# Kernel tuning notes

Measured on AMD Instinct MI355X. Metric: run time of the kernel, lower is better.

The kernel has to match this reference:

```python
import jax, jax.numpy as jnp
import numpy as np

N_HEADS = 8

def setup_inputs() -> dict:
    key = jax.random.key(0)
    kq, kk, kv = jax.random.split(key, 3)
    B, L, E = 2, 2048, 512
    return {
        "queries": jax.random.normal(kq, (B, L, E), dtype=jnp.float32),
        "keys": jax.random.normal(kk, (B, L, E), dtype=jnp.float32),
        "values": jax.random.normal(kv, (B, L, E), dtype=jnp.float32),
    }

def reference(queries, keys, values):
    B, L, E = queries.shape
    H = N_HEADS
    d = E // H
    q = queries.reshape(B, L, H, d).transpose(0, 2, 1, 3)   # [B,H,L,d]
    k = keys.reshape(B, L, H, d).transpose(0, 2, 1, 3)      # [B,H,L,d]
    v = values.reshape(B, L, H, d).transpose(0, 2, 3, 1)    # [B,H,d,L]
    # FFT cross-correlation over the channel dim (faithful to source)
    q_fft = jnp.fft.rfft(q, axis=-1)
    k_fft = jnp.fft.rfft(k, axis=-1)
    corr = jnp.fft.irfft(q_fft * jnp.conj(k_fft), n=L, axis=-1)  # [B,H,L,L]
    # time_delay_agg_training
    mean_value = jnp.mean(corr, axis=1, keepdims=True)           # [B,1,L,L]
    weights = jax.nn.softmax(corr - mean_value, axis=-1)         # [B,H,L,L]
    # V = (weights^T @ v^T)^T  -> [B,H,d,L]
    Vt = jnp.einsum('bhsl,bhds->bhdl', weights, v)
    # out = V.permute(0,2,1,3).reshape(B,L,-1)  with V=[B,H,d,L]
    out = jnp.transpose(Vt, (0, 2, 1, 3)).reshape(B, L, H * d)
    return out
```

## Files before the change

kernel.cpp:

```cpp
#include <hip/hip_runtime.h>
#include <math.h>

constexpr int CL = 2048;
constexpr int NROW = 32768;
constexpr float SCALE = 1.0f / 2048.0f;
constexpr float TWO_PI = 6.283185307179586f;

typedef short short8 __attribute__((ext_vector_type(8)));
typedef float floatx4 __attribute__((ext_vector_type(4)));

__device__ inline unsigned short f2bf(float f) {
  union { float f; unsigned u; } c; c.f = f;
  unsigned u = c.u + 0x7FFF + ((c.u >> 16) & 1);
  return (unsigned short)(u >> 16);
}
__device__ inline float bf2f(unsigned short h) {
  union { unsigned u; float f; } c; c.u = ((unsigned)h) << 16;
  return c.f;
}
__device__ inline int sw(int r, int o) {
  return r * 64 + ((((o >> 3) ^ r) & 7) << 3) + (o & 7);
}

constexpr size_t F_C0S = 0;
constexpr size_t F_C0Z = F_C0S + NROW;
constexpr size_t F_END = F_C0Z + NROW;
constexpr size_t U_CH  = 0;
constexpr size_t U_CL  = U_CH + (size_t)NROW * 64;
constexpr size_t U_BF  = U_CL + (size_t)NROW * 64;
constexpr size_t U_VF  = U_BF + (size_t)2 * 131072;
constexpr size_t BF_SPLIT = 131072;
constexpr size_t VF_PLANE = 2097152;

__launch_bounds__(256)
__global__ void mega1(const float* __restrict__ q, const float* __restrict__ kin,
                      const float* __restrict__ values,
                      unsigned short* __restrict__ Bf, unsigned short* __restrict__ Vf,
                      unsigned short* __restrict__ Ch, unsigned short* __restrict__ Cl,
                      float* __restrict__ c0s) {
  __shared__ char smem[16640];
  int tid = threadIdx.x;
  int blk = blockIdx.x;
  if (blk < 64) {
    int gid = blk * 256 + tid;
    int lt = gid >> 7, rem = gid & 127, ks = rem >> 6, lane = rem & 63;
    int qd = lane >> 4, n = lane & 15;
    int t = lt * 16 + n;
    size_t base = ((size_t)((lt * 2 + ks) * 64 + lane)) * 8;
    for (int j = 0; j < 8; ++j) {
      int kr = ks * 32 + qd * 8 + j;
      int freq = (kr < 32) ? (kr + 1) : (kr - 31);
      int ph = (freq * t) & (CL - 1);
      float ang = (float)ph * (TWO_PI / (float)CL);
      float val = (kr < 32) ? cosf(ang) : sinf(ang);
      unsigned short hi = f2bf(val);
      Bf[base + j] = hi;
      Bf[BF_SPLIT + base + j] = f2bf(val - bf2f(hi));
    }
    return;
  }
  if (blk < 576) {
    float* Vt = (float*)smem;
    int idx = blk - 64;
    int bh = idx >> 5, st = idx & 31;
    int b = bh >> 3, h = bh & 7;
    {
      int sl = tid >> 2, dq = (tid & 3) * 16;
      const float4* src = (const float4*)(values + ((size_t)(b * 2048 + st * 64 + sl)) * 512 + h * 64 + dq);
#pragma unroll
      for (int m = 0; m < 4; ++m) {
        float4 t4 = src[m];
        int base = sl * 65 + dq + m * 4;
        Vt[base] = t4.x; Vt[base + 1] = t4.y; Vt[base + 2] = t4.z; Vt[base + 3] = t4.w;
      }
    }
    __syncthreads();
#pragma unroll
    for (int iter = 0; iter < 2; ++iter) {
      int it = iter * 256 + tid;
      int lane = it & 63, ksp = (it >> 6) & 1, dt = it >> 7;
      int qd = lane >> 4, n = lane & 15;
      int d = dt * 16 + n;
      short8 hi, lo;
#pragma unroll
      for (int j = 0; j < 8; ++j) {
        float f = Vt[(ksp * 32 + qd * 8 + j) * 65 + d];
        unsigned short h2 = f2bf(f);
        hi[j] = (short)h2; lo[j] = (short)f2bf(f - bf2f(h2));
      }
      size_t off = (((size_t)(bh * 32 + st)) * 8 + dt * 2 + ksp) * 512 + lane * 8;
      *(short8*)(Vf + off) = hi;
      *(short8*)(Vf + VF_PLANE + off) = lo;
    }
    return;
  }
  unsigned short* Tws = (unsigned short*)smem;
  {
    int g0 = tid * 8;
    int lane_g = (g0 >> 3) & 63, ksp_g = (g0 >> 9) & 1, ct_g = g0 >> 10;
    int f = ct_g * 16 + (lane_g & 15);
    int cb = ksp_g * 32 + ((lane_g >> 4) & 3) * 8;
#pragma unroll
    for (int j = 0; j < 8; ++j) {
      float ang = (float)((f * (cb + j)) & 63) * (TWO_PI / 64.0f);
      float s1, c1;
      sincosf(ang, &s1, &c1);
      float re = c1, im = -s1;
      unsigned short rh = f2bf(re), ih = f2bf(im);
      Tws[g0 + j] = rh;        Tws[2048 + g0 + j] = f2bf(re - bf2f(rh));
      Tws[4096 + g0 + j] = ih; Tws[6144 + g0 + j] = f2bf(im - bf2f(ih));
    }
  }
  __syncthreads();
  int w = tid >> 6, lane = tid & 63, qd = lane >> 4, n = lane & 15;
  int blk1 = blk - 576;
  int b = blk1 >> 8, s0 = (blk1 & 255) * 8;
  int sA = s0 + w * 2 + (n >> 3), hA = n & 7;
  const float* qp = q + ((size_t)(b * 2048 + sA)) * 512 + hA * 64 + qd * 8;
  const float* kp = kin + ((size_t)(b * 2048 + sA)) * 512 + hA * 64 + qd * 8;
  float qv[16], kv[16];
#pragma unroll
  for (int ksp = 0; ksp < 2; ++ksp) {
    float4 a0 = *(const float4*)(qp + ksp * 32);
    float4 a1 = *(const float4*)(qp + ksp * 32 + 4);
    float4 b0 = *(const float4*)(kp + ksp * 32);
    float4 b1 = *(const float4*)(kp + ksp * 32 + 4);
    qv[ksp*8+0]=a0.x; qv[ksp*8+1]=a0.y; qv[ksp*8+2]=a0.z; qv[ksp*8+3]=a0.w;
    qv[ksp*8+4]=a1.x; qv[ksp*8+5]=a1.y; qv[ksp*8+6]=a1.z; qv[ksp*8+7]=a1.w;
    kv[ksp*8+0]=b0.x; kv[ksp*8+1]=b0.y; kv[ksp*8+2]=b0.z; kv[ksp*8+3]=b0.w;
    kv[ksp*8+4]=b1.x; kv[ksp*8+5]=b1.y; kv[ksp*8+6]=b1.z; kv[ksp*8+7]=b1.w;
  }
  float aq = 0.0f, ak = 0.0f;
#pragma unroll
  for (int i = 0; i < 16; ++i) {
    float sg = (i & 1) ? -1.0f : 1.0f;
    aq += sg * qv[i]; ak += sg * kv[i];
  }
  aq += __shfl_xor(aq, 16); aq += __shfl_xor(aq, 32);
  ak += __shfl_xor(ak, 16); ak += __shfl_xor(ak, 32);
  short8 Aqh[2], Aql[2], Akh[2], Akl[2];
#pragma unroll
  for (int ksp = 0; ksp < 2; ++ksp) {
#pragma unroll
    for (int j = 0; j < 8; ++j) {
      unsigned short hq = f2bf(qv[ksp*8+j]);
      Aqh[ksp][j] = (short)hq; Aql[ksp][j] = (short)f2bf(qv[ksp*8+j] - bf2f(hq));
      unsigned short hk = f2bf(kv[ksp*8+j]);
      Akh[ksp][j] = (short)hk; Akl[ksp][j] = (short)f2bf(kv[ksp*8+j] - bf2f(hk));
    }
  }
  float lmr[4] = {0,0,0,0};
  float c0v[4] = {0,0,0,0};
  int hC = (qd * 4) & 7;
  int sC = s0 + w * 2 + (qd >> 1);
#pragma unroll
  for (int ct = 0; ct < 2; ++ct) {
    short8 Brh[2], Brl[2], Bih[2], Bil[2];
#pragma unroll
    for (int ksp = 0; ksp < 2; ++ksp) {
      size_t off = (size_t)ct * 1024 + ksp * 512 + lane * 8;
      Brh[ksp] = *(const short8*)(Tws + off);
      Brl[ksp] = *(const short8*)(Tws + 2048 + off);
      Bih[ksp] = *(const short8*)(Tws + 4096 + off);
      Bil[ksp] = *(const short8*)(Tws + 6144 + off);
    }
    floatx4 qre = {0,0,0,0}, qim = {0,0,0,0}, kre = {0,0,0,0}, kim = {0,0,0,0};
#pragma unroll
    for (int ksp = 0; ksp < 2; ++ksp) {
      qre = __builtin_amdgcn_mfma_f32_16x16x32_bf16(Aqh[ksp], Brh[ksp], qre, 0,0,0);
      qre = __builtin_amdgcn_mfma_f32_16x16x32_bf16(Aqh[ksp], Brl[ksp], qre, 0,0,0);
      qre = __builtin_amdgcn_mfma_f32_16x16x32_bf16(Aql[ksp], Brh[ksp], qre, 0,0,0);
      qim = __builtin_amdgcn_mfma_f32_16x16x32_bf16(Aqh[ksp], Bih[ksp], qim, 0,0,0);
      qim = __builtin_amdgcn_mfma_f32_16x16x32_bf16(Aqh[ksp], Bil[ksp], qim, 0,0,0);
      qim = __builtin_amdgcn_mfma_f32_16x16x32_bf16(Aql[ksp], Bih[ksp], qim, 0,0,0);
      kre = __builtin_amdgcn_mfma_f32_16x16x32_bf16(Akh[ksp], Brh[ksp], kre, 0,0,0);
      kre = __builtin_amdgcn_mfma_f32_16x16x32_bf16(Akh[ksp], Brl[ksp], kre, 0,0,0);
      kre = __builtin_amdgcn_mfma_f32_16x16x32_bf16(Akl[ksp], Brh[ksp], kre, 0,0,0);
      kim = __builtin_amdgcn_mfma_f32_16x16x32_bf16(Akh[ksp], Bih[ksp], kim, 0,0,0);
      kim = __builtin_amdgcn_mfma_f32_16x16x32_bf16(Akh[ksp], Bil[ksp], kim, 0,0,0);
      kim = __builtin_amdgcn_mfma_f32_16x16x32_bf16(Akl[ksp], Bih[ksp], kim, 0,0,0);
    }
    float xre[4], xim[4], tre = 0, tim = 0;
#pragma unroll
    for (int r = 0; r < 4; ++r) {
      xre[r] = qre[r] * kre[r] + qim[r] * kim[r];
      xim[r] = qim[r] * kre[r] - qre[r] * kim[r];
      tre += xre[r]; tim += xim[r];
    }
    tre += __shfl_xor(tre, 16);
    tim += __shfl_xor(tim, 16);
    float mre = tre * 0.125f, mim = tim * 0.125f;
#pragma unroll
    for (int r = 0; r < 4; ++r) {
      float yre = xre[r] - mre, yim = xim[r] - mim;
      if (ct == 0 && n == 0) {
        c0v[r] = yre * SCALE;
      } else {
        int f = ct * 16 + n;
        float a = 2.0f * yre * SCALE, bb = -2.0f * yim * SCALE;
        size_t rowid = (size_t)((b * 8 + hC + r) * 2048 + sC);
        unsigned short ah = f2bf(a);
        Ch[rowid * 64 + f - 1] = ah;
        Cl[rowid * 64 + f - 1] = f2bf(a - bf2f(ah));
        unsigned short bh2 = f2bf(bb);
        Ch[rowid * 64 + 32 + f - 1] = bh2;
        Cl[rowid * 64 + 32 + f - 1] = f2bf(bb - bf2f(bh2));
        lmr[r] += fabsf(a) + fabsf(bb);
      }
    }
  }
  float X32 = aq * ak;
  float m32 = X32;
  m32 += __shfl_xor(m32, 1); m32 += __shfl_xor(m32, 2); m32 += __shfl_xor(m32, 4);
  float A32 = 2.0f * (X32 - m32 * 0.125f) * SCALE;
  if (qd == 0) {
    size_t rowid = (size_t)((b * 8 + (n & 7)) * 2048 + s0 + w * 2 + (n >> 3));
    unsigned short ah = f2bf(A32);
    Ch[rowid * 64 + 31] = ah;
    Cl[rowid * 64 + 31] = f2bf(A32 - bf2f(ah));
    Ch[rowid * 64 + 63] = 0;
    Cl[rowid * 64 + 63] = 0;
  }
  float absA32 = fabsf(A32);
#pragma unroll
  for (int r = 0; r < 4; ++r) {
    lmr[r] += __shfl_xor(lmr[r], 1);
    lmr[r] += __shfl_xor(lmr[r], 2);
    lmr[r] += __shfl_xor(lmr[r], 4);
    lmr[r] += __shfl_xor(lmr[r], 8);
  }
  int qb = lane & 48;
#pragma unroll
  for (int r = 0; r < 4; ++r) {
    float a32r = __shfl(absA32, qb + (qb >> 2) + r);
    if (n == 0) {
      float M = fabsf(c0v[r]) + lmr[r] + a32r;
      size_t rowid = (size_t)((b * 8 + hC + r) * 2048 + sC);
      c0s[rowid] = c0v[r] - M;
    }
  }
}

__launch_bounds__(256)
__global__ void k3_z(const unsigned short* __restrict__ Ch, const unsigned short* __restrict__ Cl,
                     const float* __restrict__ c0s, const unsigned short* __restrict__ Bf,
                     float* __restrict__ c0z) {
  __shared__ float Zl[64];
  int tid = threadIdx.x;
  int w = tid >> 6, lane = tid & 63, q = lane >> 4, n = lane & 15;
  int rowbase = blockIdx.x * 64;
  short8 Ah[4][2], Al[4][2];
#pragma unroll
  for (int c = 0; c < 4; ++c)
#pragma unroll
    for (int ksp = 0; ksp < 2; ++ksp) {
      size_t srow = (size_t)(rowbase + c * 16 + n);
      Ah[c][ksp] = *(const short8*)(Ch + srow * 64 + ksp * 32 + q * 8);
      Al[c][ksp] = *(const short8*)(Cl + srow * 64 + ksp * 32 + q * 8);
    }
  float c0r[4][4], zacc[4][4];
#pragma unroll
  for (int c = 0; c < 4; ++c)
#pragma unroll
    for (int r = 0; r < 4; ++r) {
      c0r[c][r] = c0s[rowbase + c * 16 + q * 4 + r];
      zacc[c][r] = 0.0f;
    }
  if (tid < 64) Zl[tid] = 0.0f;
  const unsigned short* BfL = Bf + BF_SPLIT;
  for (int lt = w; lt < 128; lt += 4) {
    size_t b0 = ((size_t)(lt * 2 + 0) * 64 + lane) * 8;
    size_t b1 = ((size_t)(lt * 2 + 1) * 64 + lane) * 8;
    short8 Bh0 = *(const short8*)(Bf + b0);
    short8 Bh1 = *(const short8*)(Bf + b1);
    short8 Bl0 = *(const short8*)(BfL + b0);
    short8 Bl1 = *(const short8*)(BfL + b1);
#pragma unroll
    for (int c = 0; c < 4; ++c) {
      floatx4 y = {0.f, 0.f, 0.f, 0.f};
      y = __builtin_amdgcn_mfma_f32_16x16x32_bf16(Ah[c][0], Bh0, y, 0, 0, 0);
      y = __builtin_amdgcn_mfma_f32_16x16x32_bf16(Ah[c][1], Bh1, y, 0, 0, 0);
      y = __builtin_amdgcn_mfma_f32_16x16x32_bf16(Ah[c][0], Bl0, y, 0, 0, 0);
      y = __builtin_amdgcn_mfma_f32_16x16x32_bf16(Ah[c][1], Bl1, y, 0, 0, 0);
      y = __builtin_amdgcn_mfma_f32_16x16x32_bf16(Al[c][0], Bh0, y, 0, 0, 0);
      y = __builtin_amdgcn_mfma_f32_16x16x32_bf16(Al[c][1], Bh1, y, 0, 0, 0);
#pragma unroll
      for (int r = 0; r < 4; ++r) zacc[c][r] += __expf(y[r] + c0r[c][r]);
    }
  }
  __syncthreads();
#pragma unroll
  for (int c = 0; c < 4; ++c)
#pragma unroll
    for (int r = 0; r < 4; ++r) {
#pragma unroll
      for (int m = 1; m < 16; m <<= 1) zacc[c][r] += __shfl_xor(zacc[c][r], m, 16);
      if (n == 0) atomicAdd(&Zl[c * 16 + q * 4 + r], zacc[c][r]);
    }
  __syncthreads();
  if (tid < 64) c0z[rowbase + tid] = c0s[rowbase + tid] - __logf(Zl[tid]);
}

#define K4_LOADA(st_, sl_)                                                           \
  do {                                                                               \
    int rz_ = bh * 2048 + (st_) * 64;                                                \
    size_t srow_ = (size_t)(rz_ + w * 16 + n);                                       \
    Ahs[sl_][0] = *(const short8*)(Ch + srow_ * 64 + qd * 8);                        \
    Ahs[sl_][1] = *(const short8*)(Ch + srow_ * 64 + 32 + qd * 8);                   \
    Als[sl_][0] = *(const short8*)(Cl + srow_ * 64 + qd * 8);                        \
    Als[sl_][1] = *(const short8*)(Cl + srow_ * 64 + 32 + qd * 8);                   \
    c0rs[sl_] = *(const float4*)(c0z + rz_ + w * 16 + qd * 4);                       \
  } while (0)

#define K4_LOADV(st_, sl_)                                                           \
  do {                                                                               \
    size_t vo_ = (((size_t)(bh * 32 + (st_))) * 8 + w * 2) * 512 + lane * 8;         \
    Vhs[sl_][0] = *(const short8*)(Vf + vo_);                                        \
    Vhs[sl_][1] = *(const short8*)(Vf + vo_ + 512);                                  \
    Vls[sl_][0] = *(const short8*)(VfL + vo_);                                       \
    Vls[sl_][1] = *(const short8*)(VfL + vo_ + 512);                                 \
  } while (0)

#define K4_PV(sl_)                                                                   \
  do {                                                                               \
    _Pragma("unroll")                                                                \
    for (int ksp_ = 0; ksp_ < 2; ++ksp_) {                                           \
      short8 Vh_ = Vhs[sl_][ksp_], Vl_ = Vls[sl_][ksp_];                             \
      _Pragma("unroll")                                                              \
      for (int lt_ = 0; lt_ < 4; ++lt_) {                                            \
        short8 E_ = *(const short8*)(&Es[sl_][sw(lt_ * 16 + n, ksp_ * 32 + qd * 8)]);\
        accv[lt_] = __builtin_amdgcn_mfma_f32_16x16x32_bf16(E_, Vh_, accv[lt_],0,0,0);\
        accv[lt_] = __builtin_amdgcn_mfma_f32_16x16x32_bf16(E_, Vl_, accv[lt_],0,0,0);\
      }                                                                              \
    }                                                                                \
  } while (0)

#define K4_ITER(st_, sl_, first_, last_)                                             \
  do {                                                                               \
    float4 cc_ = c0rs[sl_];                                                          \
    _Pragma("unroll")                                                                \
    for (int lt_ = 0; lt_ < 4; ++lt_) {                                              \
      floatx4 y = {0, 0, 0, 0};                                                      \
      y = __builtin_amdgcn_mfma_f32_16x16x32_bf16(Ahs[sl_][0], Bbh[lt_][0], y,0,0,0);\
      y = __builtin_amdgcn_mfma_f32_16x16x32_bf16(Ahs[sl_][1], Bbh[lt_][1], y,0,0,0);\
      y = __builtin_amdgcn_mfma_f32_16x16x32_bf16(Ahs[sl_][0], Bbl[lt_][0], y,0,0,0);\
      y = __builtin_amdgcn_mfma_f32_16x16x32_bf16(Ahs[sl_][1], Bbl[lt_][1], y,0,0,0);\
      y = __builtin_amdgcn_mfma_f32_16x16x32_bf16(Als[sl_][0], Bbh[lt_][0], y,0,0,0);\
      y = __builtin_amdgcn_mfma_f32_16x16x32_bf16(Als[sl_][1], Bbh[lt_][1], y,0,0,0);\
      unsigned short e0_ = f2bf(__expf(y[0] + cc_.x));                               \
      unsigned short e1_ = f2bf(__expf(y[1] + cc_.y));                               \
      unsigned short e2_ = f2bf(__expf(y[2] + cc_.z));                               \
      unsigned short e3_ = f2bf(__expf(y[3] + cc_.w));                               \
      uint2 p_;                                                                      \
      p_.x = (unsigned)e0_ | ((unsigned)e1_ << 16);                                  \
      p_.y = (unsigned)e2_ | ((unsigned)e3_ << 16);                                  \
      *(uint2*)(&Es[sl_][sw(lt_ * 16 + n, w * 16 + qd * 4)]) = p_;                   \
    }                                                                                \
    if (!(last_)) { K4_LOADA((st_) + 1, 1 - (sl_)); }                                \
    if (!(first_)) { K4_PV(1 - (sl_)); }                                             \
    if (!(last_)) { K4_LOADV((st_) + 1, 1 - (sl_)); }                                \
    __syncthreads();                                                                 \
  } while (0)

__launch_bounds__(256, 2)
__global__ void k4_out(const unsigned short* __restrict__ Ch, const unsigned short* __restrict__ Cl,
                       const float* __restrict__ c0z, const unsigned short* __restrict__ Bf,
                       const unsigned short* __restrict__ Vf, float* __restrict__ out) {
  __shared__ unsigned short Es[2][64 * 64];
  int tid = threadIdx.x;
  int w = tid >> 6, lane = tid & 63, qd = lane >> 4, n = lane & 15;
  int bh = blockIdx.x, b = bh >> 3, h = bh & 7;
  int l0 = blockIdx.y * 64, lt0 = blockIdx.y * 4;
  const unsigned short* BfL = Bf + BF_SPLIT;
  const unsigned short* VfL = Vf + VF_PLANE;
  short8 Bbh[4][2], Bbl[4][2];
#pragma unroll
  for (int lt = 0; lt < 4; ++lt)
#pragma unroll
    for (int ksp = 0; ksp < 2; ++ksp) {
      size_t bo = ((size_t)((lt0 + lt) * 2 + ksp) * 64 + lane) * 8;
      Bbh[lt][ksp] = *(const short8*)(Bf + bo);
      Bbl[lt][ksp] = *(const short8*)(BfL + bo);
    }
  floatx4 accv[4];
#pragma unroll
  for (int lt = 0; lt < 4; ++lt) accv[lt] = (floatx4){0.f, 0.f, 0.f, 0.f};
  short8 Ahs[2][2], Als[2][2], Vhs[2][2], Vls[2][2];
  float4 c0rs[2];
  K4_LOADA(0, 0);
  K4_LOADV(0, 0);
  K4_ITER(0, 0, true, false);
  for (int st2 = 0; st2 < 15; ++st2) {
    K4_ITER(2 * st2 + 1, 1, false, false);
    K4_ITER(2 * st2 + 2, 0, false, false);
  }
  K4_ITER(31, 1, false, true);
  K4_PV(1);
#pragma unroll
  for (int lt = 0; lt < 4; ++lt) {
    size_t base = ((size_t)((b * 64 + w * 16 + n) * 8 + h)) * 2048 + l0 + lt * 16 + qd * 4;
    float4 o4;
    o4.x = accv[lt][0]; o4.y = accv[lt][1]; o4.z = accv[lt][2]; o4.w = accv[lt][3];
    *(float4*)(out + base) = o4;
  }
}

extern "C" void kernel_launch(void* const* d_in, const int* in_sizes, int n_in,
                              void* d_out, int out_size, void* d_ws, size_t ws_size,
                              hipStream_t stream) {
  const float* q = (const float*)d_in[0];
  const float* k = (const float*)d_in[1];
  const float* v = (const float*)d_in[2];
  float* out = (float*)d_out;
  float* ws = (float*)d_ws;
  float* c0s = ws + F_C0S;
  float* c0z = ws + F_C0Z;
  unsigned short* ubase = (unsigned short*)(ws + F_END);
  unsigned short* Ch = ubase + U_CH;
  unsigned short* Cl = ubase + U_CL;
  unsigned short* Bf = ubase + U_BF;
  unsigned short* Vf = ubase + U_VF;

  mega1<<<dim3(1088), dim3(256), 0, stream>>>(q, k, v, Bf, Vf, Ch, Cl, c0s);
  k3_z<<<dim3(512), dim3(256), 0, stream>>>(Ch, Cl, c0s, Bf, c0z);
  k4_out<<<dim3(16, 32), dim3(256), 0, stream>>>(Ch, Cl, c0z, Bf, Vf, out);
}
```

Baseline: 156.6 us.

## Switch split-bf16 MFMA products to fp16 with fewer correction terms

Converts the twiddle/basis matrix, values, and exp weights from bf16 to fp16 and uses the f16 MFMA instruction. The basis and value operands lose their low correction planes, and the correlation operand keeps a hi/lo fp16 split. This cuts the MFMA count per tile from 6 to 4 in the score and normalizer stages and from 2 to 1 in the PV stage, and also reduces memory traffic. fp16 has more mantissa bits than bf16, so fewer terms are meant to hold accuracy. It risks fp16 range or precision loss on the exp weights, which are converted with round-toward-zero, and on single-plane V.

```diff
diff --git a/kernel.cpp b/kernel.cpp
--- a/kernel.cpp
+++ b/kernel.cpp
@@ -8,6 +8,8 @@
 
 typedef short short8 __attribute__((ext_vector_type(8)));
 typedef float floatx4 __attribute__((ext_vector_type(4)));
+typedef _Float16 half8 __attribute__((ext_vector_type(8)));
+typedef __fp16 fp16x2 __attribute__((ext_vector_type(2)));
 
 __device__ inline unsigned short f2bf(float f) {
   union { float f; unsigned u; } c; c.f = f;
@@ -17,6 +19,12 @@
 __device__ inline float bf2f(unsigned short h) {
   union { unsigned u; float f; } c; c.u = ((unsigned)h) << 16;
   return c.f;
+}
+__device__ inline unsigned short f2h(float f) {
+  union { _Float16 h; unsigned short u; } c; c.h = (_Float16)f; return c.u;
+}
+__device__ inline float h2f(unsigned short u) {
+  union { unsigned short u; _Float16 h; } c; c.u = u; return (float)c.h;
 }
 __device__ inline int sw(int r, int o) {
   return r * 64 + ((((o >> 3) ^ r) & 7) << 3) + (o & 7);
@@ -29,7 +37,6 @@
 constexpr size_t U_CL  = U_CH + (size_t)NROW * 64;
 constexpr size_t U_BF  = U_CL + (size_t)NROW * 64;
 constexpr size_t U_VF  = U_BF + (size_t)2 * 131072;
-constexpr size_t BF_SPLIT = 131072;
 constexpr size_t VF_PLANE = 2097152;
 
 __launch_bounds__(256)
@@ -53,9 +60,7 @@
       int ph = (freq * t) & (CL - 1);
       float ang = (float)ph * (TWO_PI / (float)CL);
       float val = (kr < 32) ? cosf(ang) : sinf(ang);
-      unsigned short hi = f2bf(val);
-      Bf[base + j] = hi;
-      Bf[BF_SPLIT + base + j] = f2bf(val - bf2f(hi));
+      Bf[base + j] = f2h(val);
     }
     return;
   }
@@ -81,16 +86,12 @@
       int lane = it & 63, ksp = (it >> 6) & 1, dt = it >> 7;
       int qd = lane >> 4, n = lane & 15;
       int d = dt * 16 + n;
-      short8 hi, lo;
-#pragma unroll
-      for (int j = 0; j < 8; ++j) {
-        float f = Vt[(ksp * 32 + qd * 8 + j) * 65 + d];
-        unsigned short h2 = f2bf(f);
-        hi[j] = (short)h2; lo[j] = (short)f2bf(f - bf2f(h2));
-      }
+      short8 hi;
+#pragma unroll
+      for (int j = 0; j < 8; ++j)
+        hi[j] = (short)f2h(Vt[(ksp * 32 + qd * 8 + j) * 65 + d]);
       size_t off = (((size_t)(bh * 32 + st)) * 8 + dt * 2 + ksp) * 512 + lane * 8;
       *(short8*)(Vf + off) = hi;
-      *(short8*)(Vf + VF_PLANE + off) = lo;
     }
     return;
   }
@@ -199,12 +200,12 @@
         int f = ct * 16 + n;
         float a = 2.0f * yre * SCALE, bb = -2.0f * yim * SCALE;
         size_t rowid = (size_t)((b * 8 + hC + r) * 2048 + sC);
-        unsigned short ah = f2bf(a);
+        unsigned short ah = f2h(a);
         Ch[rowid * 64 + f - 1] = ah;
-        Cl[rowid * 64 + f - 1] = f2bf(a - bf2f(ah));
-        unsigned short bh2 = f2bf(bb);
+        Cl[rowid * 64 + f - 1] = f2h(a - h2f(ah));
+        unsigned short bh2 = f2h(bb);
         Ch[rowid * 64 + 32 + f - 1] = bh2;
-        Cl[rowid * 64 + 32 + f - 1] = f2bf(bb - bf2f(bh2));
+        Cl[rowid * 64 + 32 + f - 1] = f2h(bb - h2f(bh2));
         lmr[r] += fabsf(a) + fabsf(bb);
       }
     }
@@ -215,9 +216,9 @@
   float A32 = 2.0f * (X32 - m32 * 0.125f) * SCALE;
   if (qd == 0) {
     size_t rowid = (size_t)((b * 8 + (n & 7)) * 2048 + s0 + w * 2 + (n >> 3));
-    unsigned short ah = f2bf(A32);
+    unsigned short ah = f2h(A32);
     Ch[rowid * 64 + 31] = ah;
-    Cl[rowid * 64 + 31] = f2bf(A32 - bf2f(ah));
+    Cl[rowid * 64 + 31] = f2h(A32 - h2f(ah));
     Ch[rowid * 64 + 63] = 0;
     Cl[rowid * 64 + 63] = 0;
   }
@@ -249,14 +250,14 @@
   int tid = threadIdx.x;
   int w = tid >> 6, lane = tid & 63, q = lane >> 4, n = lane & 15;
   int rowbase = blockIdx.x * 64;
-  short8 Ah[4][2], Al[4][2];
+  half8 Ah[4][2], Al[4][2];
 #pragma unroll
   for (int c = 0; c < 4; ++c)
 #pragma unroll
     for (int ksp = 0; ksp < 2; ++ksp) {
       size_t srow = (size_t)(rowbase + c * 16 + n);
-      Ah[c][ksp] = *(const short8*)(Ch + srow * 64 + ksp * 32 + q * 8);
-      Al[c][ksp] = *(const short8*)(Cl + srow * 64 + ksp * 32 + q * 8);
+      Ah[c][ksp] = *(const half8*)(Ch + srow * 64 + ksp * 32 + q * 8);
+      Al[c][ksp] = *(const half8*)(Cl + srow * 64 + ksp * 32 + q * 8);
     }
   float c0r[4][4], zacc[4][4];
 #pragma unroll
@@ -267,23 +268,18 @@
       zacc[c][r] = 0.0f;
     }
   if (tid < 64) Zl[tid] = 0.0f;
-  const unsigned short* BfL = Bf + BF_SPLIT;
   for (int lt = w; lt < 128; lt += 4) {
     size_t b0 = ((size_t)(lt * 2 + 0) * 64 + lane) * 8;
     size_t b1 = ((size_t)(lt * 2 + 1) * 64 + lane) * 8;
-    short8 Bh0 = *(const short8*)(Bf + b0);
-    short8 Bh1 = *(const short8*)(Bf + b1);
-    short8 Bl0 = *(const short8*)(BfL + b0);
-    short8 Bl1 = *(const short8*)(BfL + b1);
+    half8 Bh0 = *(const half8*)(Bf + b0);
+    half8 Bh1 = *(const half8*)(Bf + b1);
 #pragma unroll
     for (int c = 0; c < 4; ++c) {
       floatx4 y = {0.f, 0.f, 0.f, 0.f};
-      y = __builtin_amdgcn_mfma_f32_16x16x32_bf16(Ah[c][0], Bh0, y, 0, 0, 0);
-      y = __builtin_amdgcn_mfma_f32_16x16x32_bf16(Ah[c][1], Bh1, y, 0, 0, 0);
-      y = __builtin_amdgcn_mfma_f32_16x16x32_bf16(Ah[c][0], Bl0, y, 0, 0, 0);
-      y = __builtin_amdgcn_mfma_f32_16x16x32_bf16(Ah[c][1], Bl1, y, 0, 0, 0);
-      y = __builtin_amdgcn_mfma_f32_16x16x32_bf16(Al[c][0], Bh0, y, 0, 0, 0);
-      y = __builtin_amdgcn_mfma_f32_16x16x32_bf16(Al[c][1], Bh1, y, 0, 0, 0);
+      y = __builtin_amdgcn_mfma_f32_16x16x32_f16(Ah[c][0], Bh0, y, 0, 0, 0);
+      y = __builtin_amdgcn_mfma_f32_16x16x32_f16(Ah[c][1], Bh1, y, 0, 0, 0);
+      y = __builtin_amdgcn_mfma_f32_16x16x32_f16(Al[c][0], Bh0, y, 0, 0, 0);
+      y = __builtin_amdgcn_mfma_f32_16x16x32_f16(Al[c][1], Bh1, y, 0, 0, 0);
 #pragma unroll
       for (int r = 0; r < 4; ++r) zacc[c][r] += __expf(y[r] + c0r[c][r]);
     }
@@ -305,32 +301,29 @@
   do {                                                                               \
     int rz_ = bh * 2048 + (st_) * 64;                                                \
     size_t srow_ = (size_t)(rz_ + w * 16 + n);                                       \
-    Ahs[sl_][0] = *(const short8*)(Ch + srow_ * 64 + qd * 8);                        \
-    Ahs[sl_][1] = *(const short8*)(Ch + srow_ * 64 + 32 + qd * 8);                   \
-    Als[sl_][0] = *(const short8*)(Cl + srow_ * 64 + qd * 8);                        \
-    Als[sl_][1] = *(const short8*)(Cl + srow_ * 64 + 32 + qd * 8);                   \
+    Ahs[sl_][0] = *(const half8*)(Ch + srow_ * 64 + qd * 8);                         \
+    Ahs[sl_][1] = *(const half8*)(Ch + srow_ * 64 + 32 + qd * 8);                    \
+    Als[sl_][0] = *(const half8*)(Cl + srow_ * 64 + qd * 8);                         \
+    Als[sl_][1] = *(const half8*)(Cl + srow_ * 64 + 32 + qd * 8);                    \
     c0rs[sl_] = *(const float4*)(c0z + rz_ + w * 16 + qd * 4);                       \
   } while (0)
 
 #define K4_LOADV(st_, sl_)                                                           \
   do {                                                                               \
     size_t vo_ = (((size_t)(bh * 32 + (st_))) * 8 + w * 2) * 512 + lane * 8;         \
-    Vhs[sl_][0] = *(const short8*)(Vf + vo_);                                        \
-    Vhs[sl_][1] = *(const short8*)(Vf + vo_ + 512);                                  \
-    Vls[sl_][0] = *(const short8*)(VfL + vo_);                                       \
-    Vls[sl_][1] = *(const short8*)(VfL + vo_ + 512);                                 \
+    Vhs[sl_][0] = *(const half8*)(Vf + vo_);                                         \
+    Vhs[sl_][1] = *(const half8*)(Vf + vo_ + 512);                                   \
   } while (0)
 
 #define K4_PV(sl_)                                                                   \
   do {                                                                               \
     _Pragma("unroll")                                                                \
     for (int ksp_ = 0; ksp_ < 2; ++ksp_) {                                           \
-      short8 Vh_ = Vhs[sl_][ksp_], Vl_ = Vls[sl_][ksp_];                             \
+      half8 Vh_ = Vhs[sl_][ksp_];                                                    \
       _Pragma("unroll")                                                              \
       for (int lt_ = 0; lt_ < 4; ++lt_) {                                            \
-        short8 E_ = *(const short8*)(&Es[sl_][sw(lt_ * 16 + n, ksp_ * 32 + qd * 8)]);\
-        accv[lt_] = __builtin_amdgcn_mfma_f32_16x16x32_bf16(E_, Vh_, accv[lt_],0,0,0);\
-        accv[lt_] = __builtin_amdgcn_mfma_f32_16x16x32_bf16(E_, Vl_, accv[lt_],0,0,0);\
+        half8 E_ = *(const half8*)(&Es[sl_][sw(lt_ * 16 + n, ksp_ * 32 + qd * 8)]);  \
+        accv[lt_] = __builtin_amdgcn_mfma_f32_16x16x32_f16(E_, Vh_, accv[lt_],0,0,0);\
       }                                                                              \
     }                                                                                \
   } while (0)
@@ -341,19 +334,15 @@
     _Pragma("unroll")                                                                \
     for (int lt_ = 0; lt_ < 4; ++lt_) {                                              \
       floatx4 y = {0, 0, 0, 0};                                                      \
-      y = __builtin_amdgcn_mfma_f32_16x16x32_bf16(Ahs[sl_][0], Bbh[lt_][0], y,0,0,0);\
-      y = __builtin_amdgcn_mfma_f32_16x16x32_bf16(Ahs[sl_][1], Bbh[lt_][1], y,0,0,0);\
-      y = __builtin_amdgcn_mfma_f32_16x16x32_bf16(Ahs[sl_][0], Bbl[lt_][0], y,0,0,0);\
-      y = __builtin_amdgcn_mfma_f32_16x16x32_bf16(Ahs[sl_][1], Bbl[lt_][1], y,0,0,0);\
-      y = __builtin_amdgcn_mfma_f32_16x16x32_bf16(Als[sl_][0], Bbh[lt_][0], y,0,0,0);\
-      y = __builtin_amdgcn_mfma_f32_16x16x32_bf16(Als[sl_][1], Bbh[lt_][1], y,0,0,0);\
-      unsigned short e0_ = f2bf(__expf(y[0] + cc_.x));                               \
-      unsigned short e1_ = f2bf(__expf(y[1] + cc_.y));                               \
-      unsigned short e2_ = f2bf(__expf(y[2] + cc_.z));                               \
-      unsigned short e3_ = f2bf(__expf(y[3] + cc_.w));                               \
+      y = __builtin_amdgcn_mfma_f32_16x16x32_f16(Ahs[sl_][0], Bbh[lt_][0], y,0,0,0); \
+      y = __builtin_amdgcn_mfma_f32_16x16x32_f16(Ahs[sl_][1], Bbh[lt_][1], y,0,0,0); \
+      y = __builtin_amdgcn_mfma_f32_16x16x32_f16(Als[sl_][0], Bbh[lt_][0], y,0,0,0); \
+      y = __builtin_amdgcn_mfma_f32_16x16x32_f16(Als[sl_][1], Bbh[lt_][1], y,0,0,0); \
+      union { fp16x2 h; unsigned u; } pk0_, pk1_;                                    \
+      pk0_.h = __builtin_amdgcn_cvt_pkrtz(__expf(y[0] + cc_.x), __expf(y[1] + cc_.y));\
+      pk1_.h = __builtin_amdgcn_cvt_pkrtz(__expf(y[2] + cc_.z), __expf(y[3] + cc_.w));\
       uint2 p_;                                                                      \
-      p_.x = (unsigned)e0_ | ((unsigned)e1_ << 16);                                  \
-      p_.y = (unsigned)e2_ | ((unsigned)e3_ << 16);                                  \
+      p_.x = pk0_.u; p_.y = pk1_.u;                                                  \
       *(uint2*)(&Es[sl_][sw(lt_ * 16 + n, w * 16 + qd * 4)]) = p_;                   \
     }                                                                                \
     if (!(last_)) { K4_LOADA((st_) + 1, 1 - (sl_)); }                                \
@@ -371,21 +360,18 @@
   int w = tid >> 6, lane = tid & 63, qd = lane >> 4, n = lane & 15;
   int bh = blockIdx.x, b = bh >> 3, h = bh & 7;
   int l0 = blockIdx.y * 64, lt0 = blockIdx.y * 4;
-  const unsigned short* BfL = Bf + BF_SPLIT;
-  const unsigned short* VfL = Vf + VF_PLANE;
-  short8 Bbh[4][2], Bbl[4][2];
+  half8 Bbh[4][2];
 #pragma unroll
   for (int lt = 0; lt < 4; ++lt)
 #pragma unroll
     for (int ksp = 0; ksp < 2; ++ksp) {
       size_t bo = ((size_t)((lt0 + lt) * 2 + ksp) * 64 + lane) * 8;
-      Bbh[lt][ksp] = *(const short8*)(Bf + bo);
-      Bbl[lt][ksp] = *(const short8*)(BfL + bo);
+      Bbh[lt][ksp] = *(const half8*)(Bf + bo);
     }
   floatx4 accv[4];
 #pragma unroll
   for (int lt = 0; lt < 4; ++lt) accv[lt] = (floatx4){0.f, 0.f, 0.f, 0.f};
-  short8 Ahs[2][2], Als[2][2], Vhs[2][2], Vls[2][2];
+  half8 Ahs[2][2], Als[2][2], Vhs[2][2];
   float4 c0rs[2];
   K4_LOADA(0, 0);
   K4_LOADV(0, 0);
```

After: 141.1 us. -9.9%, faster.
